# Kernel optimization log

Hardware: AMD Instinct MI355X
Metric: run time of the kernel (lower is better)

Reference implementation:

```python
import jax, jax.numpy as jnp
from jax import lax
import numpy as np

LAMBDA_DAG = 0.5
B, C = 64, 5000
PARENT_PROB = 0.0008  # ~4 parents per GO term


def setup_inputs() -> dict:
    key = jax.random.key(0)
    k1, k2, k3 = jax.random.split(key, 3)
    logits = jax.random.normal(k1, (B, C), dtype=jnp.float32)
    # sparse multilabel targets (binary floats, like GO annotations)
    labels = (jax.random.uniform(k2, (B, C)) < 0.02).astype(jnp.float32)
    # sparse binary DAG adjacency: dag[i, j] = 1 if j is a parent of i
    dag = (jax.random.uniform(k3, (C, C)) < PARENT_PROB).astype(jnp.float32)
    dag = dag * (1.0 - jnp.eye(C, dtype=jnp.float32))  # no self-parents
    return {"logits": logits, "labels": labels, "dag_matrix": dag}


def reference(logits, labels, dag_matrix):
    # BCEWithLogitsLoss (mean): log(1 + exp(l)) - l * y, numerically stable
    bce = jnp.mean(jnp.logaddexp(0.0, logits) - logits * labels)

    probs = jax.nn.sigmoid(logits)                      # [B, C]
    mask = (dag_matrix > 0).astype(probs.dtype)          # [C, C]
    n_par = mask.sum(axis=1)                             # [C] parents per child

    # Accumulate sum over batch of relu(p_child - p_parent)^2 as a [C, C] matrix
    # via scan over the batch dim (keeps peak memory at one [C, C] tile).
    def body(acc, p):  # p: [C]
        d = jnp.maximum(p[:, None] - p[None, :], 0.0)
        return acc + d * d, None

    nterms = probs.shape[1]
    viol_sum, _ = lax.scan(body, jnp.zeros((nterms, nterms), probs.dtype), probs)

    # per-child-term mean over (batch, n_parents_i), only for terms with parents
    per_term = (viol_sum * mask).sum(axis=1)             # [C]
    batch = jnp.asarray(probs.shape[0], probs.dtype)
    term_mean = jnp.where(n_par > 0, per_term / (batch * jnp.maximum(n_par, 1.0)), 0.0)

    total_edges = mask.sum()
    dag_penalty = jnp.where(total_edges > 0, term_mean.sum() / jnp.maximum(total_edges, 1.0), 0.0)

    loss = bce + LAMBDA_DAG * dag_penalty
    return loss
```

## Files before the change

### kernel.cpp

```cpp
#include <hip/hip_runtime.h>
#include <math.h>

#define LAMBDA_DAG 0.5f

__global__ void k_probs_bce(const float* __restrict__ logits,
                            const float* __restrict__ labels,
                            float* __restrict__ pT,
                            float* __restrict__ bce_part,
                            int B, int C) {
    const int N = B * C;
    float acc = 0.f;
    for (int idx = blockIdx.x * blockDim.x + threadIdx.x; idx < N;
         idx += gridDim.x * blockDim.x) {
        float l = logits[idx];
        float y = labels[idx];
        acc += fmaxf(l, 0.f) + log1pf(expf(-fabsf(l))) - l * y;
        float p = 1.f / (1.f + expf(-l));
        int b = idx / C;
        int c = idx - b * C;
        pT[(size_t)c * B + b] = p;
    }
    __shared__ float sdata[256];
    sdata[threadIdx.x] = acc;
    __syncthreads();
    for (int s = blockDim.x >> 1; s > 0; s >>= 1) {
        if (threadIdx.x < s) sdata[threadIdx.x] += sdata[threadIdx.x + s];
        __syncthreads();
    }
    if (threadIdx.x == 0) bce_part[blockIdx.x] = sdata[0];
}

__global__ void __launch_bounds__(256) k_dag_rows(
        const float* __restrict__ dag,
        const float* __restrict__ pT,
        float* __restrict__ per_term,
        float* __restrict__ npar,
        int B, int C) {
    const int i = blockIdx.x;
    __shared__ float pi[128];
    for (int b = threadIdx.x; b < B; b += blockDim.x)
        pi[b] = pT[(size_t)i * B + b];
    __syncthreads();

    const float* drow = dag + (size_t)i * C;
    const int C4 = C >> 2;
    float psum = 0.f, pcnt = 0.f;

    const float4* drow4 = (const float4*)drow;
    for (int q = threadIdx.x; q < C4; q += blockDim.x) {
        float4 d4 = drow4[q];
        float dv[4] = {d4.x, d4.y, d4.z, d4.w};
#pragma unroll
        for (int k = 0; k < 4; ++k) {
            if (dv[k] > 0.f) {
                const int j = q * 4 + k;
                const float* pj = pT + (size_t)j * B;
                float s = 0.f;
                for (int b = 0; b < B; ++b) {
                    float diff = fmaxf(pi[b] - pj[b], 0.f);
                    s += diff * diff;
                }
                psum += s;
                pcnt += 1.f;
            }
        }
    }
    for (int j = C4 * 4 + threadIdx.x; j < C; j += blockDim.x) {
        if (drow[j] > 0.f) {
            const float* pj = pT + (size_t)j * B;
            float s = 0.f;
            for (int b = 0; b < B; ++b) {
                float diff = fmaxf(pi[b] - pj[b], 0.f);
                s += diff * diff;
            }
            psum += s;
            pcnt += 1.f;
        }
    }

    __shared__ float s1[256], s2[256];
    s1[threadIdx.x] = psum;
    s2[threadIdx.x] = pcnt;
    __syncthreads();
    for (int s = blockDim.x >> 1; s > 0; s >>= 1) {
        if (threadIdx.x < s) {
            s1[threadIdx.x] += s1[threadIdx.x + s];
            s2[threadIdx.x] += s2[threadIdx.x + s];
        }
        __syncthreads();
    }
    if (threadIdx.x == 0) {
        per_term[i] = s1[0];
        npar[i] = s2[0];
    }
}

__global__ void k_final(const float* __restrict__ per_term,
                        const float* __restrict__ npar,
                        const float* __restrict__ bce_part, int nb,
                        float* __restrict__ out, int B, int C) {
    float bs = 0.f, ps = 0.f, es = 0.f;
    for (int k = threadIdx.x; k < nb; k += blockDim.x) bs += bce_part[k];
    for (int i = threadIdx.x; i < C; i += blockDim.x) {
        float np = npar[i];
        es += np;
        if (np > 0.f) ps += per_term[i] / ((float)B * np);
    }
    __shared__ float s1[256], s2[256], s3[256];
    s1[threadIdx.x] = bs;
    s2[threadIdx.x] = ps;
    s3[threadIdx.x] = es;
    __syncthreads();
    for (int s = blockDim.x >> 1; s > 0; s >>= 1) {
        if (threadIdx.x < s) {
            s1[threadIdx.x] += s1[threadIdx.x + s];
            s2[threadIdx.x] += s2[threadIdx.x + s];
            s3[threadIdx.x] += s3[threadIdx.x + s];
        }
        __syncthreads();
    }
    if (threadIdx.x == 0) {
        float penalty = (s3[0] > 0.f) ? (s2[0] / s3[0]) : 0.f;
        out[0] = s1[0] / (float)(B * C) + LAMBDA_DAG * penalty;
    }
}

extern "C" void kernel_launch(void* const* d_in, const int* in_sizes, int n_in,
                              void* d_out, int out_size, void* d_ws, size_t ws_size,
                              hipStream_t stream) {
    const float* logits = (const float*)d_in[0];
    const float* labels = (const float*)d_in[1];
    const float* dag    = (const float*)d_in[2];
    float* out = (float*)d_out;

    const int C = (int)(sqrt((double)in_sizes[2]) + 0.5);
    const int B = in_sizes[0] / C;

    float* ws       = (float*)d_ws;
    float* pT       = ws;
    float* per_term = pT + (size_t)C * B;
    float* nparw    = per_term + C;
    float* bce_part = nparw + C;

    const int NB1 = 320;
    k_probs_bce<<<NB1, 256, 0, stream>>>(logits, labels, pT, bce_part, B, C);
    k_dag_rows<<<C, 256, 0, stream>>>(dag, pT, per_term, nparw, B, C);
    k_final<<<1, 256, 0, stream>>>(per_term, nparw, bce_part, NB1, out, B, C);
}
```

Measured before the change: 190.3 us.

## Flatten DAG scan into per-thread 32-element segments with atomic accumulation

Replaces the one-block-per-row DAG kernel with a flat kernel where each thread streams 32 contiguous adjacency entries using eight float4 loads. For each nonzero edge it computes the squared-violation sum with vectorized pT loads and atomically adds the result and a count into per-term accumulators, which the first kernel now zeroes. This targets the per-row block overhead, the shared-memory reductions and the poor load balance of the sparse 100 MB adjacency read. In exchange it adds atomics and needs the matrix size to be a multiple of 32 so the float4 segment loads stay in bounds, which 25M satisfies.

```diff
diff --git a/kernel.cpp b/kernel.cpp
--- a/kernel.cpp
+++ b/kernel.cpp
@@ -7,21 +7,27 @@
                             const float* __restrict__ labels,
                             float* __restrict__ pT,
                             float* __restrict__ bce_part,
+                            float* __restrict__ per_term,
+                            float* __restrict__ npar,
                             int B, int C) {
     const int N = B * C;
-    float acc = 0.f;
-    for (int idx = blockIdx.x * blockDim.x + threadIdx.x; idx < N;
-         idx += gridDim.x * blockDim.x) {
+    const int stride = gridDim.x * blockDim.x;
+    const int t0 = blockIdx.x * blockDim.x + threadIdx.x;
+
+    for (int i = t0; i < C; i += stride) { per_term[i] = 0.f; npar[i] = 0.f; }
+
+    float accv = 0.f;
+    for (int idx = t0; idx < N; idx += stride) {
         float l = logits[idx];
         float y = labels[idx];
-        acc += fmaxf(l, 0.f) + log1pf(expf(-fabsf(l))) - l * y;
+        accv += fmaxf(l, 0.f) + log1pf(expf(-fabsf(l))) - l * y;
         float p = 1.f / (1.f + expf(-l));
         int b = idx / C;
         int c = idx - b * C;
         pT[(size_t)c * B + b] = p;
     }
     __shared__ float sdata[256];
-    sdata[threadIdx.x] = acc;
+    sdata[threadIdx.x] = accv;
     __syncthreads();
     for (int s = blockDim.x >> 1; s > 0; s >>= 1) {
         if (threadIdx.x < s) sdata[threadIdx.x] += sdata[threadIdx.x + s];
@@ -30,68 +36,55 @@
     if (threadIdx.x == 0) bce_part[blockIdx.x] = sdata[0];
 }
 
-__global__ void __launch_bounds__(256) k_dag_rows(
+__global__ void __launch_bounds__(256) k_dag_flat(
         const float* __restrict__ dag,
         const float* __restrict__ pT,
         float* __restrict__ per_term,
         float* __restrict__ npar,
-        int B, int C) {
-    const int i = blockIdx.x;
-    __shared__ float pi[128];
-    for (int b = threadIdx.x; b < B; b += blockDim.x)
-        pi[b] = pT[(size_t)i * B + b];
-    __syncthreads();
+        int B, int C, int nseg) {
+    const int seg = blockIdx.x * blockDim.x + threadIdx.x;
+    if (seg >= nseg) return;
+    const int base = seg * 32;
+    const float4* dp = (const float4*)(dag + (size_t)base);
 
-    const float* drow = dag + (size_t)i * C;
-    const int C4 = C >> 2;
-    float psum = 0.f, pcnt = 0.f;
+    float4 v[8];
+#pragma unroll
+    for (int h = 0; h < 8; ++h) v[h] = dp[h];
 
-    const float4* drow4 = (const float4*)drow;
-    for (int q = threadIdx.x; q < C4; q += blockDim.x) {
-        float4 d4 = drow4[q];
-        float dv[4] = {d4.x, d4.y, d4.z, d4.w};
+    const int B4 = B >> 2;
 #pragma unroll
-        for (int k = 0; k < 4; ++k) {
-            if (dv[k] > 0.f) {
-                const int j = q * 4 + k;
-                const float* pj = pT + (size_t)j * B;
-                float s = 0.f;
-                for (int b = 0; b < B; ++b) {
-                    float diff = fmaxf(pi[b] - pj[b], 0.f);
-                    s += diff * diff;
+    for (int h = 0; h < 8; ++h) {
+        float4 d4 = v[h];
+        float g = d4.x + d4.y + d4.z + d4.w;
+        if (g > 0.f) {
+#pragma unroll
+            for (int k = 0; k < 4; ++k) {
+                float dv = (k == 0) ? d4.x : (k == 1) ? d4.y : (k == 2) ? d4.z : d4.w;
+                if (dv > 0.f) {
+                    int f = base + h * 4 + k;
+                    int i = f / C;
+                    int j = f - i * C;
+                    const float4* pi4 = (const float4*)(pT + (size_t)i * B);
+                    const float4* pj4 = (const float4*)(pT + (size_t)j * B);
+                    float s = 0.f;
+                    for (int q = 0; q < B4; ++q) {
+                        float4 a = pi4[q];
+                        float4 b = pj4[q];
+                        float d0 = fmaxf(a.x - b.x, 0.f);
+                        float d1 = fmaxf(a.y - b.y, 0.f);
+                        float d2 = fmaxf(a.z - b.z, 0.f);
+                        float d3 = fmaxf(a.w - b.w, 0.f);
+                        s += d0 * d0 + d1 * d1 + d2 * d2 + d3 * d3;
+                    }
+                    for (int b = B4 * 4; b < B; ++b) {
+                        float diff = fmaxf(pT[(size_t)i * B + b] - pT[(size_t)j * B + b], 0.f);
+                        s += diff * diff;
+                    }
+                    atomicAdd(&per_term[i], s);
+                    atomicAdd(&npar[i], 1.f);
                 }
-                psum += s;
-                pcnt += 1.f;
             }
         }
-    }
-    for (int j = C4 * 4 + threadIdx.x; j < C; j += blockDim.x) {
-        if (drow[j] > 0.f) {
-            const float* pj = pT + (size_t)j * B;
-            float s = 0.f;
-            for (int b = 0; b < B; ++b) {
-                float diff = fmaxf(pi[b] - pj[b], 0.f);
-                s += diff * diff;
-            }
-            psum += s;
-            pcnt += 1.f;
-        }
-    }
-
-    __shared__ float s1[256], s2[256];
-    s1[threadIdx.x] = psum;
-    s2[threadIdx.x] = pcnt;
-    __syncthreads();
-    for (int s = blockDim.x >> 1; s > 0; s >>= 1) {
-        if (threadIdx.x < s) {
-            s1[threadIdx.x] += s1[threadIdx.x + s];
-            s2[threadIdx.x] += s2[threadIdx.x + s];
-        }
-        __syncthreads();
-    }
-    if (threadIdx.x == 0) {
-        per_term[i] = s1[0];
-        npar[i] = s2[0];
     }
 }
 
@@ -135,15 +128,21 @@
 
     const int C = (int)(sqrt((double)in_sizes[2]) + 0.5);
     const int B = in_sizes[0] / C;
+    const int CC = in_sizes[2];
 
     float* ws       = (float*)d_ws;
     float* pT       = ws;
     float* per_term = pT + (size_t)C * B;
     float* nparw    = per_term + C;
     float* bce_part = nparw + C;
+    const int NB1 = 320;
 
-    const int NB1 = 320;
-    k_probs_bce<<<NB1, 256, 0, stream>>>(logits, labels, pT, bce_part, B, C);
-    k_dag_rows<<<C, 256, 0, stream>>>(dag, pT, per_term, nparw, B, C);
+    k_probs_bce<<<NB1, 256, 0, stream>>>(logits, labels, pT, bce_part,
+                                         per_term, nparw, B, C);
+
+    const int nseg = (CC + 31) / 32;
+    const int nblk = (nseg + 255) / 256;
+    k_dag_flat<<<nblk, 256, 0, stream>>>(dag, pT, per_term, nparw, B, C, nseg);
+
     k_final<<<1, 256, 0, stream>>>(per_term, nparw, bce_part, NB1, out, B, C);
 }
```

Result: slower. 195.3 us (+2.6%).
